# Kernel tuning notes

Measured on AMD Instinct MI355X. Metric: run time of the kernel, lower is better.

The kernel has to match this reference:

```python
import jax, jax.numpy as jnp
import numpy as np

C = 64
HIMG = 256
WIMG = 256
N = HIMG * WIMG
E = 8 * N
HEADS = 4
DHEAD = C // HEADS
NMOD = 9   # 9 GraphAttentionModules (c1_1..c3_3)
NLAY = 3   # layers per module
NSTACK = 2 # RBS1, RBS2
NBLK = 4   # resblocks per stack


def setup_inputs() -> dict:
    key = jax.random.key(0)
    ks = jax.random.split(key, 12)
    s = 0.05
    x = jax.random.normal(ks[0], (1, C, HIMG, WIMG), dtype=jnp.float32)
    edge_index = jax.random.randint(ks[1], (2, E), 0, N, dtype=jnp.int32)
    gat_Wl = jax.random.normal(ks[2], (NMOD, NLAY, C, C), dtype=jnp.float32) * s
    gat_Wr = jax.random.normal(ks[3], (NMOD, NLAY, C, C), dtype=jnp.float32) * s
    gat_att = jax.random.normal(ks[4], (NMOD, NLAY, HEADS, DHEAD), dtype=jnp.float32) * s
    gat_b = jax.random.normal(ks[5], (NMOD, NLAY, C), dtype=jnp.float32) * s
    cc_w = jax.random.normal(ks[6], (3, C, 3 * C), dtype=jnp.float32) * s
    cc_b = jax.random.normal(ks[7], (3, C), dtype=jnp.float32) * s
    rb_w = jax.random.normal(ks[8], (NSTACK, NBLK, 2, C, C, 3, 3), dtype=jnp.float32) * s
    rb_b = jax.random.normal(ks[9], (NSTACK, NBLK, 2, C), dtype=jnp.float32) * s
    rb_a = jnp.full((NSTACK, NBLK), 0.25, dtype=jnp.float32)  # PReLU init
    return dict(x=x, edge_index=edge_index, gat_Wl=gat_Wl, gat_Wr=gat_Wr,
                gat_att=gat_att, gat_b=gat_b, cc_w=cc_w, cc_b=cc_b,
                rb_w=rb_w, rb_b=rb_b, rb_a=rb_a)


def _gatv2(x, src, dst, Wl, Wr, att, b):
    # x: [N,C]; GATv2Conv (PyG): xl = lin_l(x) (source msgs), xr = lin_r(x) (target)
    xl = (x @ Wl).reshape(-1, HEADS, DHEAD)
    xr = (x @ Wr).reshape(-1, HEADS, DHEAD)
    xj = xl[src]                               # [E,H,D] source
    xi = xr[dst]                               # [E,H,D] target
    e = jax.nn.leaky_relu(xi + xj, 0.2)        # [E,H,D]
    logits = jnp.einsum('ehd,hd->eh', e, att)  # [E,H]
    m = jax.ops.segment_max(logits, dst, num_segments=N)
    m = jnp.where(jnp.isfinite(m), m, 0.0)
    ex = jnp.exp(logits - m[dst])
    den = jax.ops.segment_sum(ex, dst, num_segments=N)
    alpha = ex / (den[dst] + 1e-16)            # edge softmax per target node
    out = jax.ops.segment_sum(xj * alpha[..., None], dst, num_segments=N)
    return out.reshape(-1, C) + b


def _gam(xn, src, dst, m, gat_Wl, gat_Wr, gat_att, gat_b):
    # GraphAttentionModule: 3 GAT layers, each followed by ELU
    for l in range(NLAY):
        xn = jax.nn.elu(_gatv2(xn, src, dst, gat_Wl[m, l], gat_Wr[m, l],
                               gat_att[m, l], gat_b[m, l]))
    return xn


def _to_nodes(img):   # [1,C,H,W] -> [N,C]
    return img[0].transpose(1, 2, 0).reshape(N, C)


def _to_img(xn):      # [N,C] -> [1,C,H,W]
    return xn.reshape(HIMG, WIMG, C).transpose(2, 0, 1)[None]


def _conv3(x, w, b):
    y = jax.lax.conv_general_dilated(x, w, (1, 1), 'SAME',
                                     dimension_numbers=('NCHW', 'OIHW', 'NCHW'))
    return y + b[None, :, None, None]


def _resblocks(x, w, b, a):
    # stack of 4 ResBlocks: conv3 -> PReLU -> conv3, res_scale=1
    for i in range(NBLK):
        h = _conv3(x, w[i, 0], b[i, 0])
        h = jnp.where(h >= 0, h, a[i] * h)  # PReLU (single shared param)
        h = _conv3(h, w[i, 1], b[i, 1])
        x = x + h
    return x


def _stage(img, midx, ci, src, dst, gat_Wl, gat_Wr, gat_att, gat_b, cc_w, cc_b):
    xn = _to_nodes(img)
    branches = [_to_img(_gam(xn, src, dst, m, gat_Wl, gat_Wr, gat_att, gat_b))
                for m in midx]
    cat = jnp.concatenate(branches, axis=1)            # [1,3C,H,W]
    out = jnp.einsum('oc,bchw->bohw', cc_w[ci], cat) + cc_b[ci][None, :, None, None]
    return out + img


def reference(x, edge_index, gat_Wl, gat_Wr, gat_att, gat_b, cc_w, cc_b,
              rb_w, rb_b, rb_a):
    src, dst = edge_index[0], edge_index[1]
    out = _stage(x, (0, 1, 2), 0, src, dst, gat_Wl, gat_Wr, gat_att, gat_b, cc_w, cc_b)
    out = _resblocks(out, rb_w[0], rb_b[0], rb_a[0])
    out = _stage(out, (3, 4, 5), 1, src, dst, gat_Wl, gat_Wr, gat_att, gat_b, cc_w, cc_b)
    out = _resblocks(out, rb_w[1], rb_b[1], rb_a[1])
    out = _stage(out, (6, 7, 8), 2, src, dst, gat_Wl, gat_Wr, gat_att, gat_b, cc_w, cc_b)
    return out
```

## Files before the change

### kernel.cpp

```cpp
#include <hip/hip_runtime.h>
#include <hip/hip_bf16.h>
#include <math.h>

#define N_NODES 65536
#define HW      65536
#define NE      524288
#define NC      (N_NODES * 64)

typedef __bf16 bf16x8 __attribute__((ext_vector_type(8)));
typedef float  f32x4  __attribute__((ext_vector_type(4)));
typedef float  f32x2  __attribute__((ext_vector_type(2)));
typedef int    i32x4  __attribute__((ext_vector_type(4)));
typedef unsigned int uint2v __attribute__((ext_vector_type(2)));

static __device__ __forceinline__ f32x4 mfma16(bf16x8 a, bf16x8 b, f32x4 c) {
    return __builtin_amdgcn_mfma_f32_16x16x32_bf16(a, b, c, 0, 0, 0);
}

static __device__ __forceinline__ unsigned short f2bs(float f) {
    return __builtin_bit_cast(unsigned short, __float2bfloat16(f));
}

__global__ void k_hist(const int* __restrict__ dstA, int* __restrict__ cnt) {
    int e = blockIdx.x * 256 + threadIdx.x;
    if (e < NE) atomicAdd(&cnt[dstA[e]], 1);
}

__global__ void k_scan(const int* __restrict__ cnt, int* __restrict__ off) {
    __shared__ int sums[1024];
    int t = threadIdx.x;
    int base = t * 64;
    int s = 0;
    for (int i = 0; i < 64; ++i) s += cnt[base + i];
    sums[t] = s;
    __syncthreads();
    for (int d = 1; d < 1024; d <<= 1) {
        int v = (t >= d) ? sums[t - d] : 0;
        __syncthreads();
        sums[t] += v;
        __syncthreads();
    }
    int run = sums[t] - s;
    for (int i = 0; i < 64; ++i) { off[base + i] = run; run += cnt[base + i]; }
    if (t == 1023) off[N_NODES] = run;
}

__global__ void k_fill(const int* __restrict__ srcA, const int* __restrict__ dstA,
                       int* __restrict__ cur, int* __restrict__ csr) {
    int e = blockIdx.x * 256 + threadIdx.x;
    if (e < NE) {
        int p = atomicAdd(&cur[dstA[e]], 1);
        csr[p] = srcA[e];
    }
}

__global__ void k_bsort(const int* __restrict__ off, int* __restrict__ bperm) {
    __shared__ int degs[256];
    int n = blockIdx.x * 256 + threadIdx.x;
    int deg = off[n + 1] - off[n];
    degs[threadIdx.x] = deg;
    __syncthreads();
    int base32 = threadIdx.x & ~31;
    int i = threadIdx.x & 31;
    int rank = 0;
#pragma unroll
    for (int j = 0; j < 32; ++j) {
        int dj = degs[base32 + j];
        rank += (dj > deg) || (dj == deg && j < i);
    }
    bperm[(n & ~31) + rank] = i;
}

__global__ void k_cvpack(const float* __restrict__ w, __hip_bfloat16* __restrict__ d) {
    int idx = blockIdx.x * 256 + threadIdx.x;
    if (idx >= 589824) return;
    int j = idx & 7, lane = (idx >> 3) & 63, r = idx >> 9;
    int kk = r & 1; r >>= 1;
    int nt = r & 3; r >>= 2;
    int tap = r % 9, cv = r / 9;
    int co = nt * 16 + (lane & 15);
    int ci = kk * 32 + (lane >> 4) * 8 + j;
    d[idx] = __float2bfloat16(w[((cv * 64 + co) * 64 + ci) * 9 + tap]);
}

__global__ void k_mmpack(const float* __restrict__ Wl, const float* __restrict__ Wr,
                         __hip_bfloat16* __restrict__ d) {
    int idx = blockIdx.x * 256 + threadIdx.x;
    if (idx >= 221184) return;
    int j = idx & 7, lane = (idx >> 3) & 63, r = idx >> 9;
    int kk = r & 1; r >>= 1;
    int nt = r & 3; r >>= 2;
    int side = r & 1, lay = r >> 1;
    int co = nt * 16 + (lane & 15);
    int ci = kk * 32 + (lane >> 4) * 8 + j;
    const float* W = side ? Wr : Wl;
    d[idx] = __float2bfloat16(W[lay * 4096 + ci * 64 + co]);
}

__global__ void k_ccpack(const float* __restrict__ w, __hip_bfloat16* __restrict__ d) {
    int idx = blockIdx.x * 256 + threadIdx.x;
    if (idx >= 36864) return;
    int j = idx & 7;
    int u = idx >> 3;
    int lane = u & 63;
    int f = (u >> 6) & 7;
    int sb = u >> 9;
    int kk = f & 1, nt = f >> 1;
    int br = sb % 3, st = sb / 3;
    int k = br * 64 + kk * 32 + (lane >> 4) * 8 + j;
    int co = nt * 16 + (lane & 15);
    d[idx] = __float2bfloat16(w[st * 12288 + co * 192 + k]);
}

__global__ void k_init(const float* __restrict__ img, float* __restrict__ xn,
                       __hip_bfloat16* __restrict__ xb) {
    __shared__ float tile[64][65];
    int nb = blockIdx.x * 64;
    for (int idx = threadIdx.x; idx < 4096; idx += 256) {
        int c = idx >> 6, n = idx & 63;
        tile[c][n] = img[c * HW + nb + n];
    }
    __syncthreads();
    for (int idx = threadIdx.x; idx < 4096; idx += 256) {
        int n = idx >> 6, c = idx & 63;
        float v = tile[c][n];
        xn[(nb + n) * 64 + c] = v;
        xb[(nb + n) * 64 + c] = __float2bfloat16(v);
    }
}

static __device__ __forceinline__ void mm_phase32(char* smem, int t,
        const __hip_bfloat16* __restrict__ pwm, unsigned char* __restrict__ xlo,
        __hip_bfloat16* __restrict__ xrb, int n0) {
    i32x4* la = (i32x4*)smem;
    int lane = t & 63, side = t >> 6;
    const i32x4* wpt = (const i32x4*)pwm + side * 512 + lane;
    f32x4 acc[2][4];
#pragma unroll
    for (int mi = 0; mi < 2; ++mi)
#pragma unroll
        for (int nt = 0; nt < 4; ++nt) acc[mi][nt] = (f32x4)0.0f;
    bf16x8 b[4][2];
#pragma unroll
    for (int nt = 0; nt < 4; ++nt)
#pragma unroll
        for (int kk = 0; kk < 2; ++kk)
            b[nt][kk] = __builtin_bit_cast(bf16x8, wpt[(nt * 2 + kk) * 64]);
#pragma unroll
    for (int mi = 0; mi < 2; ++mi) {
        int row = mi * 16 + (lane & 15);
#pragma unroll
        for (int kk = 0; kk < 2; ++kk) {
            bf16x8 a = __builtin_bit_cast(bf16x8,
                la[row * 8 + (((kk << 2) | (lane >> 4)) ^ (row & 7))]);
#pragma unroll
            for (int nt = 0; nt < 4; ++nt)
                acc[mi][nt] = mfma16(a, b[nt][kk], acc[mi][nt]);
        }
    }
    __syncthreads();
    unsigned short* ls = (unsigned short*)smem;
    if (side == 0) {
#pragma unroll
        for (int mi = 0; mi < 2; ++mi)
#pragma unroll
            for (int nt = 0; nt < 4; ++nt) {
                int co = nt * 16 + (lane & 15);
#pragma unroll
                for (int r = 0; r < 4; ++r) {
                    int row = mi * 16 + (lane >> 4) * 4 + r;
                    ls[row * 68 + co] = f2bs(acc[mi][nt][r]);
                }
            }
    } else {
#pragma unroll
        for (int mi = 0; mi < 2; ++mi)
#pragma unroll
            for (int nt = 0; nt < 4; ++nt) {
                int co = nt * 16 + (lane & 15);
#pragma unroll
                for (int r = 0; r < 4; ++r) {
                    int node = n0 + mi * 16 + (lane >> 4) * 4 + r;
                    xrb[(size_t)node * 64 + co] = __float2bfloat16(acc[mi][nt][r]);
                }
            }
    }
    __syncthreads();
    for (int u = t; u < 256; u += 128) {
        int node = u >> 3, oct = u & 7;
        const unsigned short* p = ls + node * 68 + oct * 8;
        uint2v w0 = *(const uint2v*)p;
        uint2v w1 = *(const uint2v*)(p + 4);
        float f0 = __builtin_bit_cast(float, w0[0] << 16);
        float f1 = __builtin_bit_cast(float, w0[0] & 0xffff0000u);
        float f2 = __builtin_bit_cast(float, w0[1] << 16);
        float f3 = __builtin_bit_cast(float, w0[1] & 0xffff0000u);
        float f4 = __builtin_bit_cast(float, w1[0] << 16);
        float f5 = __builtin_bit_cast(float, w1[0] & 0xffff0000u);
        float f6 = __builtin_bit_cast(float, w1[1] << 16);
        float f7 = __builtin_bit_cast(float, w1[1] & 0xffff0000u);
        int v0 = 0, v1 = 0;
        v0 = __builtin_amdgcn_cvt_pk_fp8_f32(f0, f1, v0, false);
        v0 = __builtin_amdgcn_cvt_pk_fp8_f32(f2, f3, v0, true);
        v1 = __builtin_amdgcn_cvt_pk_fp8_f32(f4, f5, v1, false);
        v1 = __builtin_amdgcn_cvt_pk_fp8_f32(f6, f7, v1, true);
        uint2v o;
        o[0] = (unsigned)v0;
        o[1] = (unsigned)v1;
        *(uint2v*)(xlo + (size_t)(n0 + node) * 64 + oct * 8) = o;
    }
}

static __device__ __forceinline__ uint2v gat_node(
        const unsigned char* __restrict__ xl8, const __hip_bfloat16* __restrict__ xrb,
        const int* __restrict__ csr, const int* __restrict__ csr_c, int cbase, int cc,
        int n, int e0, int e1, int c4, f32x2 a01, f32x2 a23, f32x4 b4) {
    uint2v xw = *(const uint2v*)(xrb + (size_t)n * 64 + c4);
    f32x2 xi01, xi23;
    xi01[0] = __builtin_bit_cast(float, xw[0] << 16);
    xi01[1] = __builtin_bit_cast(float, xw[0] & 0xffff0000u);
    xi23[0] = __builtin_bit_cast(float, xw[1] << 16);
    xi23[1] = __builtin_bit_cast(float, xw[1] & 0xffff0000u);
    float s = 0.f;
    f32x2 acc01 = {0.f, 0.f}, acc23 = {0.f, 0.f};
    int rounds = (e1 - e0 + 1) >> 1;
    int e = e0;
    for (int i = 0; i < rounds; ++i, e += 2) {
        bool aB = (e + 1) < e1;
        int eB = aB ? e + 1 : e;
        int rA = e - cbase, rB = eB - cbase;
        int sA = (rA < cc) ? csr_c[rA] : csr[e];
        int sB = (rB < cc) ? csr_c[rB] : csr[eB];
        unsigned int wA = *(const unsigned int*)(xl8 + (size_t)sA * 64 + c4);
        unsigned int wB = *(const unsigned int*)(xl8 + (size_t)sB * 64 + c4);
        f32x2 xjA01 = __builtin_amdgcn_cvt_pk_f32_fp8((int)wA, false);
        f32x2 xjA23 = __builtin_amdgcn_cvt_pk_f32_fp8((int)wA, true);
        f32x2 xjB01 = __builtin_amdgcn_cvt_pk_f32_fp8((int)wB, false);
        f32x2 xjB23 = __builtin_amdgcn_cvt_pk_f32_fp8((int)wB, true);
        f32x2 vA01 = xi01 + xjA01;
        f32x2 vA23 = xi23 + xjA23;
        vA01 = __builtin_elementwise_max(vA01, vA01 * 0.2f);
        vA23 = __builtin_elementwise_max(vA23, vA23 * 0.2f);
        f32x2 pA2 = vA01 * a01 + vA23 * a23;
        float pA = pA2[0] + pA2[1];
        f32x2 vB01 = xi01 + xjB01;
        f32x2 vB23 = xi23 + xjB23;
        vB01 = __builtin_elementwise_max(vB01, vB01 * 0.2f);
        vB23 = __builtin_elementwise_max(vB23, vB23 * 0.2f);
        f32x2 pB2 = vB01 * a01 + vB23 * a23;
        float pB = pB2[0] + pB2[1];
        pA += __shfl_xor(pA, 1);
        pA += __shfl_xor(pA, 2);
        pB += __shfl_xor(pB, 1);
        pB += __shfl_xor(pB, 2);
        float exA = exp2f(fmaxf(pA, -100.f));
        float exB = exp2f(fmaxf(pB, -100.f));
        exB = aB ? exB : 0.f;
        s += exA + exB;
        acc01 = acc01 + exA * xjA01 + exB * xjB01;
        acc23 = acc23 + exA * xjA23 + exB * xjB23;
    }
    float inv = __builtin_amdgcn_rcpf(s + 1e-16f);
    float v0 = fmaf(acc01[0], inv, b4[0]);
    float v1 = fmaf(acc01[1], inv, b4[1]);
    float v2 = fmaf(acc23[0], inv, b4[2]);
    float v3 = fmaf(acc23[1], inv, b4[3]);
    v0 = v0 > 0.f ? v0 : __expf(v0) - 1.f;
    v1 = v1 > 0.f ? v1 : __expf(v1) - 1.f;
    v2 = v2 > 0.f ? v2 : __expf(v2) - 1.f;
    v3 = v3 > 0.f ? v3 : __expf(v3) - 1.f;
    uint2v o;
    o[0] = (unsigned)f2bs(v0) | ((unsigned)f2bs(v1) << 16);
    o[1] = (unsigned)f2bs(v2) | ((unsigned)f2bs(v3) << 16);
    return o;
}

__global__ __launch_bounds__(128) void k_mm3(const __hip_bfloat16* __restrict__ Xb,
        const __hip_bfloat16* __restrict__ pw, unsigned char* __restrict__ XL8,
        __hip_bfloat16* __restrict__ XRb) {
    __shared__ i32x4 smem4[272];
    char* smem = (char*)smem4;
    i32x4* la = (i32x4*)smem;
    int t = threadIdx.x;
    int m = blockIdx.x >> 11;
    int n0 = (blockIdx.x & 2047) << 5;
    const i32x4* Xg = (const i32x4*)Xb + n0 * 8;
    for (int idx = t; idx < 256; idx += 128) {
        int r = idx >> 3, c = idx & 7;
        la[r * 8 + (c ^ (r & 7))] = Xg[idx];
    }
    __syncthreads();
    mm_phase32(smem, t, pw + m * 24576, XL8 + (size_t)m * NC,
               XRb + (size_t)m * NC, n0);
}

__global__ __launch_bounds__(128) void k_fuse(
        const unsigned char* __restrict__ XL8in, unsigned char* __restrict__ XL8out,
        __hip_bfloat16* __restrict__ XRb, const float* __restrict__ gatt,
        const float* __restrict__ gb, const __hip_bfloat16* __restrict__ pw,
        const int* __restrict__ off, const int* __restrict__ csr,
        const int* __restrict__ bperm) {
    __shared__ i32x4 smem4[272];
    __shared__ int csr_c[384];
    char* smem = (char*)smem4;
    int t = threadIdx.x;
    int p = blockIdx.x;
    int vi = (p & 7) * 768 + (p >> 3);
    int m = vi >> 11;
    int n0 = (vi & 2047) << 5;
    const unsigned char* xl8 = XL8in + (size_t)m * NC;
    unsigned char* xlo = XL8out + (size_t)m * NC;
    __hip_bfloat16* xrb = XRb + (size_t)m * NC;
    int cbase = off[n0];
    int cc = min(off[n0 + 32] - cbase, 384);
    for (int i = t; i < cc; i += 128) csr_c[i] = csr[cbase + i];
    __syncthreads();
    int g16 = t >> 4;
    int c4 = (t & 15) << 2;
    const float* at = gatt + m * 192;
    const float* bb = gb + m * 192;
    const float LOG2E = 1.44269504089f;
    f32x4 a4 = *(const f32x4*)(at + c4);
    f32x2 a01 = {a4[0] * LOG2E, a4[1] * LOG2E};
    f32x2 a23 = {a4[2] * LOG2E, a4[3] * LOG2E};
    f32x4 b4 = *(const f32x4*)(bb + c4);
    uint2v* lau = (uint2v*)smem;
    int cchunk = c4 >> 3, half = (c4 >> 2) & 1;
    const int* bp = bperm + n0;
#pragma unroll
    for (int nn = 0; nn < 4; ++nn) {
        int rank = (nn & 1) ? (nn * 8 + (7 - g16)) : (nn * 8 + g16);
        int r = bp[rank];
        int n = n0 + r;
        uint2v o = gat_node(xl8, xrb, csr, csr_c, cbase, cc, n,
                            off[n], off[n + 1], c4, a01, a23, b4);
        lau[(r * 8 + (cchunk ^ (r & 7))) * 2 + half] = o;
    }
    __syncthreads();
    mm_phase32(smem, t, pw + m * 24576, xlo, xrb, n0);
}

__global__ __launch_bounds__(256) void k_gatfin(const unsigned char* __restrict__ XL8,
        const __hip_bfloat16* __restrict__ XRb, const float* __restrict__ gatt,
        const float* __restrict__ gb, const int* __restrict__ off,
        const int* __restrict__ csr, __hip_bfloat16* __restrict__ brs,
        const int* __restrict__ bperm) {
    __shared__ int csr_c[320];
    int t = threadIdx.x, lane = t & 63;
    int p = blockIdx.x;
    int vi = (p & 7) * 768 + (p >> 3);
    int m = vi >> 11;
    int nblk = (vi & 2047) * 32;
    const unsigned char* xl8 = XL8 + (size_t)m * NC;
    const __hip_bfloat16* xrb = XRb + (size_t)m * NC;
    __hip_bfloat16* outb = brs + (size_t)m * NC;
    int cbase = off[nblk];
    int cc = min(off[nblk + 32] - cbase, 320);
    for (int i = t; i < cc; i += 256) csr_c[i] = csr[cbase + i];
    __syncthreads();
    int g = (lane >> 4) & 3;
    int gg = (t >> 6) * 4 + g;
    int c4 = (lane & 15) << 2;
    const float* at = gatt + m * 192;
    const float* bb = gb + m * 192;
    const float LOG2E = 1.44269504089f;
    f32x4 a4 = *(const f32x4*)(at + c4);
    f32x2 a01 = {a4[0] * LOG2E, a4[1] * LOG2E};
    f32x2 a23 = {a4[2] * LOG2E, a4[3] * LOG2E};
    f32x4 b4 = *(const f32x4*)(bb + c4);
    const int* bp = bperm + nblk;
#pragma unroll
    for (int nn = 0; nn < 2; ++nn) {
        int rank = (nn & 1) ? (16 + (15 - gg)) : gg;
        int n = nblk + bp[rank];
        uint2v o = gat_node(xl8, xrb, csr, csr_c, cbase, cc, n,
                            off[n], off[n + 1], c4, a01, a23, b4);
        *(uint2v*)(outb + (size_t)n * 64 + c4) = o;
    }
}

__global__ __launch_bounds__(256) void k_cc2(const __hip_bfloat16* __restrict__ b0,
        const __hip_bfloat16* __restrict__ b1, const __hip_bfloat16* __restrict__ b2,
        const __hip_bfloat16* __restrict__ pw, const float* __restrict__ bias,
        const float* __restrict__ resin, float* __restrict__ imgout,
        __hip_bfloat16* __restrict__ outb) {
    __shared__ i32x4 la[128 * 8];
    int t = threadIdx.x, lane = t & 63, wid = t >> 6;
    int n0 = blockIdx.x * 128;
    const __hip_bfloat16* brs[3] = {b0, b1, b2};
    const i32x4* wp4 = (const i32x4*)pw;
    f32x4 acc[2][4];
#pragma unroll
    for (int mi = 0; mi < 2; ++mi)
#pragma unroll
        for (int nt = 0; nt < 4; ++nt) acc[mi][nt] = (f32x4)0.0f;
#pragma unroll
    for (int br = 0; br < 3; ++br) {
        __syncthreads();
        const i32x4* Bg = (const i32x4*)brs[br] + n0 * 8;
        for (int idx = t; idx < 1024; idx += 256) {
            int r = idx >> 3, c = idx & 7;
            la[r * 8 + (c ^ (r & 7))] = Bg[idx];
        }
        __syncthreads();
        bf16x8 bf[4][2];
#pragma unroll
        for (int nt = 0; nt < 4; ++nt)
#pragma unroll
            for (int kk = 0; kk < 2; ++kk)
                bf[nt][kk] = __builtin_bit_cast(bf16x8,
                    wp4[(br * 8 + nt * 2 + kk) * 64 + lane]);
#pragma unroll
        for (int mi = 0; mi < 2; ++mi) {
            int row = wid * 32 + mi * 16 + (lane & 15);
#pragma unroll
            for (int kk = 0; kk < 2; ++kk) {
                bf16x8 a = __builtin_bit_cast(bf16x8,
                    la[row * 8 + (((kk << 2) | (lane >> 4)) ^ (row & 7))]);
#pragma unroll
                for (int nt = 0; nt < 4; ++nt)
                    acc[mi][nt] = mfma16(a, bf[nt][kk], acc[mi][nt]);
            }
        }
    }
#pragma unroll
    for (int mi = 0; mi < 2; ++mi)
#pragma unroll
        for (int nt = 0; nt < 4; ++nt) {
            int co = nt * 16 + (lane & 15);
            float bv = bias[co];
#pragma unroll
            for (int r = 0; r < 4; ++r) {
                int node = n0 + wid * 32 + mi * 16 + (lane >> 4) * 4 + r;
                float v = acc[mi][nt][r] + bv + resin[node * 64 + co];
                imgout[node * 64 + co] = v;
                outb[node * 64 + co] = __float2bfloat16(v);
            }
        }
}

__global__ __launch_bounds__(256) void k_ccfin(const __hip_bfloat16* __restrict__ b0,
        const __hip_bfloat16* __restrict__ b1, const __hip_bfloat16* __restrict__ b2,
        const __hip_bfloat16* __restrict__ pw, const float* __restrict__ bias,
        const float* __restrict__ resin, float* __restrict__ outp) {
    __shared__ i32x4 la[128 * 8];
    __shared__ float tt[64][132];
    int t = threadIdx.x, lane = t & 63, wid = t >> 6;
    int n0 = blockIdx.x * 128;
    const __hip_bfloat16* brs[3] = {b0, b1, b2};
    const i32x4* wp4 = (const i32x4*)pw;
    f32x4 acc[2][4];
#pragma unroll
    for (int mi = 0; mi < 2; ++mi)
#pragma unroll
        for (int nt = 0; nt < 4; ++nt) acc[mi][nt] = (f32x4)0.0f;
#pragma unroll
    for (int br = 0; br < 3; ++br) {
        __syncthreads();
        const i32x4* Bg = (const i32x4*)brs[br] + n0 * 8;
        for (int idx = t; idx < 1024; idx += 256) {
            int r = idx >> 3, c = idx & 7;
            la[r * 8 + (c ^ (r & 7))] = Bg[idx];
        }
        __syncthreads();
        bf16x8 bf[4][2];
#pragma unroll
        for (int nt = 0; nt < 4; ++nt)
#pragma unroll
            for (int kk = 0; kk < 2; ++kk)
                bf[nt][kk] = __builtin_bit_cast(bf16x8,
                    wp4[(br * 8 + nt * 2 + kk) * 64 + lane]);
#pragma unroll
        for (int mi = 0; mi < 2; ++mi) {
            int row = wid * 32 + mi * 16 + (lane & 15);
#pragma unroll
            for (int kk = 0; kk < 2; ++kk) {
                bf16x8 a = __builtin_bit_cast(bf16x8,
                    la[row * 8 + (((kk << 2) | (lane >> 4)) ^ (row & 7))]);
#pragma unroll
                for (int nt = 0; nt < 4; ++nt)
                    acc[mi][nt] = mfma16(a, bf[nt][kk], acc[mi][nt]);
            }
        }
    }
#pragma unroll
    for (int mi = 0; mi < 2; ++mi)
#pragma unroll
        for (int nt = 0; nt < 4; ++nt) {
            int co = nt * 16 + (lane & 15);
            float bv = bias[co];
#pragma unroll
            for (int r = 0; r < 4; ++r) {
                int nl = wid * 32 + mi * 16 + (lane >> 4) * 4 + r;
                tt[co][nl] = acc[mi][nt][r] + bv + resin[(n0 + nl) * 64 + co];
            }
        }
    __syncthreads();
    for (int u = t; u < 2048; u += 256) {
        int row = u >> 5;
        int col = (u & 31) * 4;
        f32x4 v = *(const f32x4*)&tt[row][col];
        *(f32x4*)(outp + row * HW + n0 + col) = v;
    }
}

template <int MODE>
__global__ __launch_bounds__(256) void k_conv(const __hip_bfloat16* __restrict__ inb,
        const __hip_bfloat16* __restrict__ wp, const float* __restrict__ bias,
        const float* __restrict__ pa, float* __restrict__ img,
        __hip_bfloat16* __restrict__ outb) {
    __shared__ i32x4 la[2][66 * 8];
    int t = threadIdx.x, lane = t & 63, wid = t >> 6;
    int y = blockIdx.x >> 2, x0 = (blockIdx.x & 3) << 6;
    f32x4 acc[4];
#pragma unroll
    for (int nt = 0; nt < 4; ++nt) acc[nt] = (f32x4)0.0f;
    const i32x4* ing = (const i32x4*)inb;
    auto stage = [&](int dy, int buf) {
        int sy = y + dy - 1;
        bool rowok = (sy >= 0) && (sy < 256);
        for (int idx = t; idx < 528; idx += 256) {
            int r = idx >> 3, c = idx & 7;
            int sx = x0 - 1 + r;
            i32x4 v = (i32x4)0;
            if (rowok && sx >= 0 && sx < 256) v = ing[(sy * 256 + sx) * 8 + c];
            la[buf][r * 8 + (c ^ (r & 7))] = v;
        }
    };
    stage(0, 0);
    __syncthreads();
#pragma unroll
    for (int dy = 0; dy < 3; ++dy) {
        if (dy < 2) stage(dy + 1, (dy + 1) & 1);
        const i32x4* lb = la[dy & 1];
#pragma unroll
        for (int dx = 0; dx < 3; ++dx) {
            const i32x4* wpt = (const i32x4*)wp + (dy * 3 + dx) * 512 + lane;
            bf16x8 b[4][2];
#pragma unroll
            for (int nt = 0; nt < 4; ++nt)
#pragma unroll
                for (int kk = 0; kk < 2; ++kk)
                    b[nt][kk] = __builtin_bit_cast(bf16x8, wpt[(nt * 2 + kk) * 64]);
            int row = dx + wid * 16 + (lane & 15);
#pragma unroll
            for (int kk = 0; kk < 2; ++kk) {
                bf16x8 a = __builtin_bit_cast(bf16x8,
                    lb[row * 8 + (((kk << 2) | (lane >> 4)) ^ (row & 7))]);
#pragma unroll
                for (int nt = 0; nt < 4; ++nt)
                    acc[nt] = mfma16(a, b[nt][kk], acc[nt]);
            }
        }
        __syncthreads();
    }
    int pbase = y * 256 + x0 + wid * 16 + (lane >> 4) * 4;
    float aprelu = (MODE == 0) ? pa[0] : 0.f;
#pragma unroll
    for (int nt = 0; nt < 4; ++nt) {
        int co = nt * 16 + (lane & 15);
        float bv = bias[co];
#pragma unroll
        for (int r = 0; r < 4; ++r) {
            int pix = pbase + r;
            float v = acc[nt][r] + bv;
            if (MODE == 0) {
                v = v >= 0.f ? v : aprelu * v;
                outb[pix * 64 + co] = __float2bfloat16(v);
            } else {
                v += img[pix * 64 + co];
                img[pix * 64 + co] = v;
                outb[pix * 64 + co] = __float2bfloat16(v);
            }
        }
    }
}

extern "C" void kernel_launch(void* const* d_in, const int* in_sizes, int n_in,
                              void* d_out, int out_size, void* d_ws, size_t ws_size,
                              hipStream_t stream) {
    const float* x    = (const float*)d_in[0];
    const int*   ei   = (const int*)d_in[1];
    const float* gWl  = (const float*)d_in[2];
    const float* gWr  = (const float*)d_in[3];
    const float* gatt = (const float*)d_in[4];
    const float* gb   = (const float*)d_in[5];
    const float* ccw  = (const float*)d_in[6];
    const float* ccb  = (const float*)d_in[7];
    const float* rbw  = (const float*)d_in[8];
    const float* rbb  = (const float*)d_in[9];
    const float* rba  = (const float*)d_in[10];
    float* outp = (float*)d_out;

    float* wsf = (float*)d_ws;
    float* xn  = wsf;
    float* img = xn + NC;
    __hip_bfloat16* xrb3 = (__hip_bfloat16*)(img + NC);
    unsigned char* xl8p0 = (unsigned char*)(xrb3 + 3 * (size_t)NC);
    unsigned char* xl8p1 = xl8p0 + 3 * (size_t)NC;
    __hip_bfloat16* xb   = (__hip_bfloat16*)(xl8p1 + 3 * (size_t)NC);
    __hip_bfloat16* b0b  = xb + NC;
    __hip_bfloat16* b1b  = b0b + NC;
    __hip_bfloat16* b2b  = b1b + NC;
    __hip_bfloat16* cvb  = b0b;
    __hip_bfloat16* wpkc = b2b + NC;
    __hip_bfloat16* wpkm = wpkc + 589824;
    __hip_bfloat16* ccpk = wpkm + 221184;
    int* ioff = (int*)(ccpk + 36864);
    int* icnt = ioff + (N_NODES + 1);
    int* icur = icnt + N_NODES;
    int* icsr = icur + N_NODES;
    int* ibperm = icsr + NE;

    const int* srcA = ei;
    const int* dstA = ei + NE;

    hipMemsetAsync(icnt, 0, N_NODES * sizeof(int), stream);
    k_hist<<<NE / 256, 256, 0, stream>>>(dstA, icnt);
    k_scan<<<1, 1024, 0, stream>>>(icnt, ioff);
    hipMemcpyAsync(icur, ioff, N_NODES * sizeof(int), hipMemcpyDeviceToDevice, stream);
    k_fill<<<NE / 256, 256, 0, stream>>>(srcA, dstA, icur, icsr);
    k_bsort<<<N_NODES / 256, 256, 0, stream>>>(ioff, ibperm);
    k_cvpack<<<2304, 256, 0, stream>>>(rbw, wpkc);
    k_mmpack<<<864, 256, 0, stream>>>(gWl, gWr, wpkm);
    k_ccpack<<<144, 256, 0, stream>>>(ccw, ccpk);
    k_init<<<1024, 256, 0, stream>>>(x, xn, xb);

    for (int st = 0; st < 3; ++st) {
        int L = st * 9;
        k_mm3<<<6144, 128, 0, stream>>>(xb, wpkm + (size_t)L * 8192, xl8p0, xrb3);
        k_fuse<<<6144, 128, 0, stream>>>(xl8p0, xl8p1, xrb3,
            gatt + L * 64, gb + L * 64, wpkm + (size_t)(L + 1) * 8192, ioff, icsr,
            ibperm);
        k_fuse<<<6144, 128, 0, stream>>>(xl8p1, xl8p0, xrb3,
            gatt + (L + 1) * 64, gb + (L + 1) * 64, wpkm + (size_t)(L + 2) * 8192,
            ioff, icsr, ibperm);
        k_gatfin<<<6144, 256, 0, stream>>>(xl8p0, xrb3,
            gatt + (L + 2) * 64, gb + (L + 2) * 64, ioff, icsr, b0b, ibperm);
        const float* resin = (st == 0) ? xn : img;
        if (st == 2) {
            k_ccfin<<<N_NODES / 128, 256, 0, stream>>>(b0b, b1b, b2b,
                ccpk + 2 * 12288, ccb + 128, resin, outp);
        } else {
            k_cc2<<<N_NODES / 128, 256, 0, stream>>>(b0b, b1b, b2b,
                ccpk + st * 12288, ccb + st * 64, resin, img, xb);
            for (int bk = 0; bk < 4; ++bk) {
                int cv = (st * 4 + bk) * 2;
                k_conv<0><<<1024, 256, 0, stream>>>(xb, wpkc + (size_t)cv * 36864,
                    rbb + cv * 64, rba + st * 4 + bk, nullptr, cvb);
                k_conv<1><<<1024, 256, 0, stream>>>(cvb, wpkc + (size_t)(cv + 1) * 36864,
                    rbb + (cv + 1) * 64, nullptr, img, xb);
            }
        }
    }
}
```

Before: 902.1 us.

## Fuse final GAT layer of all three branches with concat-conv 1x1 projection

Replaces the separate final-layer GAT kernel (one module per block) and the concat 1x1 conv kernels with one kernel. Each block handles 16 nodes across all three modules, reusing each edge's source index for three gathers. It stages the three ELU'd outputs in shared memory and immediately applies the 192->64 MFMA projection with bias and residual. This avoids writing and re-reading three bf16 branch buffers and cuts launches. The cost is more registers per thread, less parallelism per block, and strided transposed output stores in the final stage.

```diff
diff --git a/kernel.cpp b/kernel.cpp
--- a/kernel.cpp
+++ b/kernel.cpp
@@ -340,167 +340,141 @@
     mm_phase32(smem, t, pw + m * 24576, xlo, xrb, n0);
 }
 
-__global__ __launch_bounds__(256) void k_gatfin(const unsigned char* __restrict__ XL8,
-        const __hip_bfloat16* __restrict__ XRb, const float* __restrict__ gatt,
-        const float* __restrict__ gb, const int* __restrict__ off,
-        const int* __restrict__ csr, __hip_bfloat16* __restrict__ brs,
-        const int* __restrict__ bperm) {
-    __shared__ int csr_c[320];
-    int t = threadIdx.x, lane = t & 63;
+template <int FINAL>
+__global__ __launch_bounds__(256) void k_gatcc(
+        const unsigned char* __restrict__ XL8, const __hip_bfloat16* __restrict__ XRb,
+        const float* __restrict__ gatt, const float* __restrict__ gb,
+        const __hip_bfloat16* __restrict__ ccw, const float* __restrict__ ccbias,
+        const int* __restrict__ off, const int* __restrict__ csr,
+        const int* __restrict__ bperm, const float* __restrict__ resin,
+        float* __restrict__ imgout, __hip_bfloat16* __restrict__ outb,
+        float* __restrict__ outp) {
+    __shared__ int csr_c[384];
+    __shared__ int nid[16];
+    __shared__ i32x4 la[16 * 24];
+    int t = threadIdx.x;
     int p = blockIdx.x;
-    int vi = (p & 7) * 768 + (p >> 3);
-    int m = vi >> 11;
-    int nblk = (vi & 2047) * 32;
-    const unsigned char* xl8 = XL8 + (size_t)m * NC;
-    const __hip_bfloat16* xrb = XRb + (size_t)m * NC;
-    __hip_bfloat16* outb = brs + (size_t)m * NC;
-    int cbase = off[nblk];
-    int cc = min(off[nblk + 32] - cbase, 320);
+    int vi = (p & 7) * 512 + (p >> 3);
+    int base32 = (vi >> 1) << 5;
+    int half16 = vi & 1;
+    int cbase = off[base32];
+    int cc = min(off[base32 + 32] - cbase, 384);
     for (int i = t; i < cc; i += 256) csr_c[i] = csr[cbase + i];
-    __syncthreads();
-    int g = (lane >> 4) & 3;
-    int gg = (t >> 6) * 4 + g;
-    int c4 = (lane & 15) << 2;
-    const float* at = gatt + m * 192;
-    const float* bb = gb + m * 192;
+    if (t < 16) nid[t] = base32 + bperm[base32 + half16 * 16 + t];
+    __syncthreads();
+    int g = t >> 4;
+    int c4 = (t & 15) << 2;
+    int n = nid[g];
+    int e0 = off[n], e1 = off[n + 1];
     const float LOG2E = 1.44269504089f;
-    f32x4 a4 = *(const f32x4*)(at + c4);
-    f32x2 a01 = {a4[0] * LOG2E, a4[1] * LOG2E};
-    f32x2 a23 = {a4[2] * LOG2E, a4[3] * LOG2E};
-    f32x4 b4 = *(const f32x4*)(bb + c4);
-    const int* bp = bperm + nblk;
-#pragma unroll
-    for (int nn = 0; nn < 2; ++nn) {
-        int rank = (nn & 1) ? (16 + (15 - gg)) : gg;
-        int n = nblk + bp[rank];
-        uint2v o = gat_node(xl8, xrb, csr, csr_c, cbase, cc, n,
-                            off[n], off[n + 1], c4, a01, a23, b4);
-        *(uint2v*)(outb + (size_t)n * 64 + c4) = o;
-    }
-}
-
-__global__ __launch_bounds__(256) void k_cc2(const __hip_bfloat16* __restrict__ b0,
-        const __hip_bfloat16* __restrict__ b1, const __hip_bfloat16* __restrict__ b2,
-        const __hip_bfloat16* __restrict__ pw, const float* __restrict__ bias,
-        const float* __restrict__ resin, float* __restrict__ imgout,
-        __hip_bfloat16* __restrict__ outb) {
-    __shared__ i32x4 la[128 * 8];
-    int t = threadIdx.x, lane = t & 63, wid = t >> 6;
-    int n0 = blockIdx.x * 128;
-    const __hip_bfloat16* brs[3] = {b0, b1, b2};
-    const i32x4* wp4 = (const i32x4*)pw;
-    f32x4 acc[2][4];
-#pragma unroll
-    for (int mi = 0; mi < 2; ++mi)
-#pragma unroll
-        for (int nt = 0; nt < 4; ++nt) acc[mi][nt] = (f32x4)0.0f;
-#pragma unroll
-    for (int br = 0; br < 3; ++br) {
-        __syncthreads();
-        const i32x4* Bg = (const i32x4*)brs[br] + n0 * 8;
-        for (int idx = t; idx < 1024; idx += 256) {
-            int r = idx >> 3, c = idx & 7;
-            la[r * 8 + (c ^ (r & 7))] = Bg[idx];
+    f32x2 a01[3], a23[3];
+    f32x4 b4[3];
+    f32x2 xi01[3], xi23[3];
+    float s[3];
+    f32x2 ac01[3], ac23[3];
+#pragma unroll
+    for (int m = 0; m < 3; ++m) {
+        f32x4 a4 = *(const f32x4*)(gatt + m * 192 + c4);
+        a01[m][0] = a4[0] * LOG2E; a01[m][1] = a4[1] * LOG2E;
+        a23[m][0] = a4[2] * LOG2E; a23[m][1] = a4[3] * LOG2E;
+        b4[m] = *(const f32x4*)(gb + m * 192 + c4);
+        uint2v xw = *(const uint2v*)(XRb + (size_t)m * NC + (size_t)n * 64 + c4);
+        xi01[m][0] = __builtin_bit_cast(float, xw[0] << 16);
+        xi01[m][1] = __builtin_bit_cast(float, xw[0] & 0xffff0000u);
+        xi23[m][0] = __builtin_bit_cast(float, xw[1] << 16);
+        xi23[m][1] = __builtin_bit_cast(float, xw[1] & 0xffff0000u);
+        s[m] = 0.f;
+        ac01[m][0] = 0.f; ac01[m][1] = 0.f;
+        ac23[m][0] = 0.f; ac23[m][1] = 0.f;
+    }
+    int rounds = (e1 - e0 + 1) >> 1;
+    int e = e0;
+    for (int i = 0; i < rounds; ++i, e += 2) {
+        bool aB = (e + 1) < e1;
+        int eB = aB ? e + 1 : e;
+        int rA = e - cbase, rB = eB - cbase;
+        int sA = (rA < cc) ? csr_c[rA] : csr[e];
+        int sB = (rB < cc) ? csr_c[rB] : csr[eB];
+        size_t oA = (size_t)sA * 64 + c4, oB = (size_t)sB * 64 + c4;
+#pragma unroll
+        for (int m = 0; m < 3; ++m) {
+            unsigned int wA = *(const unsigned int*)(XL8 + (size_t)m * NC + oA);
+            unsigned int wB = *(const unsigned int*)(XL8 + (size_t)m * NC + oB);
+            f32x2 xjA01 = __builtin_amdgcn_cvt_pk_f32_fp8((int)wA, false);
+            f32x2 xjA23 = __builtin_amdgcn_cvt_pk_f32_fp8((int)wA, true);
+            f32x2 xjB01 = __builtin_amdgcn_cvt_pk_f32_fp8((int)wB, false);
+            f32x2 xjB23 = __builtin_amdgcn_cvt_pk_f32_fp8((int)wB, true);
+            f32x2 vA01 = xi01[m] + xjA01;
+            f32x2 vA23 = xi23[m] + xjA23;
+            vA01 = __builtin_elementwise_max(vA01, vA01 * 0.2f);
+            vA23 = __builtin_elementwise_max(vA23, vA23 * 0.2f);
+            f32x2 pA2 = vA01 * a01[m] + vA23 * a23[m];
+            float pA = pA2[0] + pA2[1];
+            f32x2 vB01 = xi01[m] + xjB01;
+            f32x2 vB23 = xi23[m] + xjB23;
+            vB01 = __builtin_elementwise_max(vB01, vB01 * 0.2f);
+            vB23 = __builtin_elementwise_max(vB23, vB23 * 0.2f);
+            f32x2 pB2 = vB01 * a01[m] + vB23 * a23[m];
+            float pB = pB2[0] + pB2[1];
+            pA += __shfl_xor(pA, 1);
+            pA += __shfl_xor(pA, 2);
+            pB += __shfl_xor(pB, 1);
+            pB += __shfl_xor(pB, 2);
+            float exA = exp2f(fmaxf(pA, -100.f));
+            float exB = exp2f(fmaxf(pB, -100.f));
+            exB = aB ? exB : 0.f;
+            s[m] += exA + exB;
+            ac01[m] = ac01[m] + exA * xjA01 + exB * xjB01;
+            ac23[m] = ac23[m] + exA * xjA23 + exB * xjB23;
         }
-        __syncthreads();
-        bf16x8 bf[4][2];
-#pragma unroll
-        for (int nt = 0; nt < 4; ++nt)
-#pragma unroll
-            for (int kk = 0; kk < 2; ++kk)
-                bf[nt][kk] = __builtin_bit_cast(bf16x8,
-                    wp4[(br * 8 + nt * 2 + kk) * 64 + lane]);
-#pragma unroll
-        for (int mi = 0; mi < 2; ++mi) {
-            int row = wid * 32 + mi * 16 + (lane & 15);
-#pragma unroll
-            for (int kk = 0; kk < 2; ++kk) {
-                bf16x8 a = __builtin_bit_cast(bf16x8,
-                    la[row * 8 + (((kk << 2) | (lane >> 4)) ^ (row & 7))]);
-#pragma unroll
-                for (int nt = 0; nt < 4; ++nt)
-                    acc[mi][nt] = mfma16(a, bf[nt][kk], acc[mi][nt]);
-            }
+    }
+    uint2v* lau = (uint2v*)la;
+#pragma unroll
+    for (int m = 0; m < 3; ++m) {
+        float inv = __builtin_amdgcn_rcpf(s[m] + 1e-16f);
+        float v0 = fmaf(ac01[m][0], inv, b4[m][0]);
+        float v1 = fmaf(ac01[m][1], inv, b4[m][1]);
+        float v2 = fmaf(ac23[m][0], inv, b4[m][2]);
+        float v3 = fmaf(ac23[m][1], inv, b4[m][3]);
+        v0 = v0 > 0.f ? v0 : __expf(v0) - 1.f;
+        v1 = v1 > 0.f ? v1 : __expf(v1) - 1.f;
+        v2 = v2 > 0.f ? v2 : __expf(v2) - 1.f;
+        v3 = v3 > 0.f ? v3 : __expf(v3) - 1.f;
+        uint2v o;
+        o[0] = (unsigned)f2bs(v0) | ((unsigned)f2bs(v1) << 16);
+        o[1] = (unsigned)f2bs(v2) | ((unsigned)f2bs(v3) << 16);
+        int ch = m * 8 + (c4 >> 3);
+        int swz = (ch & 24) | ((ch & 7) ^ (g & 7));
+        lau[(g * 24 + swz) * 2 + ((c4 >> 2) & 1)] = o;
+    }
+    __syncthreads();
+    int lane = t & 63, w = t >> 6;
+    f32x4 acc = (f32x4)0.0f;
+    const i32x4* wp4 = (const i32x4*)ccw;
+#pragma unroll
+    for (int kkg = 0; kkg < 6; ++kkg) {
+        int br = kkg >> 1, kk2 = kkg & 1;
+        bf16x8 bfr = __builtin_bit_cast(bf16x8,
+            wp4[(br * 8 + w * 2 + kk2) * 64 + lane]);
+        int row = lane & 15;
+        int ch = kkg * 4 + (lane >> 4);
+        int swz = (ch & 24) | ((ch & 7) ^ (row & 7));
+        bf16x8 afr = __builtin_bit_cast(bf16x8, la[row * 24 + swz]);
+        acc = mfma16(afr, bfr, acc);
+    }
+    int co = w * 16 + (lane & 15);
+    float bv = ccbias[co];
+#pragma unroll
+    for (int r = 0; r < 4; ++r) {
+        int row = (lane >> 4) * 4 + r;
+        int nn = nid[row];
+        float v = acc[r] + bv + resin[(size_t)nn * 64 + co];
+        if (FINAL) {
+            outp[(size_t)co * HW + nn] = v;
+        } else {
+            imgout[(size_t)nn * 64 + co] = v;
+            outb[(size_t)nn * 64 + co] = __float2bfloat16(v);
         }
-    }
-#pragma unroll
-    for (int mi = 0; mi < 2; ++mi)
-#pragma unroll
-        for (int nt = 0; nt < 4; ++nt) {
-            int co = nt * 16 + (lane & 15);
-            float bv = bias[co];
-#pragma unroll
-            for (int r = 0; r < 4; ++r) {
-                int node = n0 + wid * 32 + mi * 16 + (lane >> 4) * 4 + r;
-                float v = acc[mi][nt][r] + bv + resin[node * 64 + co];
-                imgout[node * 64 + co] = v;
-                outb[node * 64 + co] = __float2bfloat16(v);
-            }
-        }
-}
-
-__global__ __launch_bounds__(256) void k_ccfin(const __hip_bfloat16* __restrict__ b0,
-        const __hip_bfloat16* __restrict__ b1, const __hip_bfloat16* __restrict__ b2,
-        const __hip_bfloat16* __restrict__ pw, const float* __restrict__ bias,
-        const float* __restrict__ resin, float* __restrict__ outp) {
-    __shared__ i32x4 la[128 * 8];
-    __shared__ float tt[64][132];
-    int t = threadIdx.x, lane = t & 63, wid = t >> 6;
-    int n0 = blockIdx.x * 128;
-    const __hip_bfloat16* brs[3] = {b0, b1, b2};
-    const i32x4* wp4 = (const i32x4*)pw;
-    f32x4 acc[2][4];
-#pragma unroll
-    for (int mi = 0; mi < 2; ++mi)
-#pragma unroll
-        for (int nt = 0; nt < 4; ++nt) acc[mi][nt] = (f32x4)0.0f;
-#pragma unroll
-    for (int br = 0; br < 3; ++br) {
-        __syncthreads();
-        const i32x4* Bg = (const i32x4*)brs[br] + n0 * 8;
-        for (int idx = t; idx < 1024; idx += 256) {
-            int r = idx >> 3, c = idx & 7;
-            la[r * 8 + (c ^ (r & 7))] = Bg[idx];
-        }
-        __syncthreads();
-        bf16x8 bf[4][2];
-#pragma unroll
-        for (int nt = 0; nt < 4; ++nt)
-#pragma unroll
-            for (int kk = 0; kk < 2; ++kk)
-                bf[nt][kk] = __builtin_bit_cast(bf16x8,
-                    wp4[(br * 8 + nt * 2 + kk) * 64 + lane]);
-#pragma unroll
-        for (int mi = 0; mi < 2; ++mi) {
-            int row = wid * 32 + mi * 16 + (lane & 15);
-#pragma unroll
-            for (int kk = 0; kk < 2; ++kk) {
-                bf16x8 a = __builtin_bit_cast(bf16x8,
-                    la[row * 8 + (((kk << 2) | (lane >> 4)) ^ (row & 7))]);
-#pragma unroll
-                for (int nt = 0; nt < 4; ++nt)
-                    acc[mi][nt] = mfma16(a, bf[nt][kk], acc[mi][nt]);
-            }
-        }
-    }
-#pragma unroll
-    for (int mi = 0; mi < 2; ++mi)
-#pragma unroll
-        for (int nt = 0; nt < 4; ++nt) {
-            int co = nt * 16 + (lane & 15);
-            float bv = bias[co];
-#pragma unroll
-            for (int r = 0; r < 4; ++r) {
-                int nl = wid * 32 + mi * 16 + (lane >> 4) * 4 + r;
-                tt[co][nl] = acc[mi][nt][r] + bv + resin[(n0 + nl) * 64 + co];
-            }
-        }
-    __syncthreads();
-    for (int u = t; u < 2048; u += 256) {
-        int row = u >> 5;
-        int col = (u & 31) * 4;
-        f32x4 v = *(const f32x4*)&tt[row][col];
-        *(f32x4*)(outp + row * HW + n0 + col) = v;
     }
 }
 
@@ -599,11 +573,8 @@
     unsigned char* xl8p0 = (unsigned char*)(xrb3 + 3 * (size_t)NC);
     unsigned char* xl8p1 = xl8p0 + 3 * (size_t)NC;
     __hip_bfloat16* xb   = (__hip_bfloat16*)(xl8p1 + 3 * (size_t)NC);
-    __hip_bfloat16* b0b  = xb + NC;
-    __hip_bfloat16* b1b  = b0b + NC;
-    __hip_bfloat16* b2b  = b1b + NC;
-    __hip_bfloat16* cvb  = b0b;
-    __hip_bfloat16* wpkc = b2b + NC;
+    __hip_bfloat16* cvb  = xb + NC;
+    __hip_bfloat16* wpkc = cvb + NC;
     __hip_bfloat16* wpkm = wpkc + 589824;
     __hip_bfloat16* ccpk = wpkm + 221184;
     int* ioff = (int*)(ccpk + 36864);
@@ -635,15 +606,15 @@
         k_fuse<<<6144, 128, 0, stream>>>(xl8p1, xl8p0, xrb3,
             gatt + (L + 1) * 64, gb + (L + 1) * 64, wpkm + (size_t)(L + 2) * 8192,
             ioff, icsr, ibperm);
-        k_gatfin<<<6144, 256, 0, stream>>>(xl8p0, xrb3,
-            gatt + (L + 2) * 64, gb + (L + 2) * 64, ioff, icsr, b0b, ibperm);
         const float* resin = (st == 0) ? xn : img;
         if (st == 2) {
-            k_ccfin<<<N_NODES / 128, 256, 0, stream>>>(b0b, b1b, b2b,
-                ccpk + 2 * 12288, ccb + 128, resin, outp);
+            k_gatcc<1><<<4096, 256, 0, stream>>>(xl8p0, xrb3,
+                gatt + (L + 2) * 64, gb + (L + 2) * 64, ccpk + 2 * 12288, ccb + 128,
+                ioff, icsr, ibperm, resin, nullptr, nullptr, outp);
         } else {
-            k_cc2<<<N_NODES / 128, 256, 0, stream>>>(b0b, b1b, b2b,
-                ccpk + st * 12288, ccb + st * 64, resin, img, xb);
+            k_gatcc<0><<<4096, 256, 0, stream>>>(xl8p0, xrb3,
+                gatt + (L + 2) * 64, gb + (L + 2) * 64, ccpk + st * 12288,
+                ccb + st * 64, ioff, icsr, ibperm, resin, img, xb, nullptr);
             for (int bk = 0; bk < 4; ++bk) {
                 int cv = (st * 4 + bk) * 2;
                 k_conv<0><<<1024, 256, 0, stream>>>(xb, wpkc + (size_t)cv * 36864,
```

Measured after the change: 912.7 us. About the same (+1.2%).
